# Optimization experiments

Measured on AMD Instinct MI355X. Metric: run time of the kernel, lower is better.

Reference implementation:

```python
import jax, jax.numpy as jnp
import numpy as np

N = 50000        # nodes
E = 1600000      # edges (avg degree 32)
F_IN = 128
F_OUT = 128


def setup_inputs() -> dict:
    key = jax.random.key(0)
    k = jax.random.split(key, 6)
    h = jax.random.normal(k[0], (N, F_IN), dtype=jnp.float32)
    edge_feat = jax.random.normal(k[1], (E,), dtype=jnp.float32)
    src = jax.random.randint(k[2], (E,), 0, N, dtype=jnp.int32)
    dst = jax.random.randint(k[3], (E,), 0, N, dtype=jnp.int32)
    # xavier_uniform with gain=1.414 over fan_in=F_IN, fan_out=F_OUT
    limit = 1.414 * np.sqrt(6.0 / (F_IN + F_OUT))
    weight = jax.random.uniform(k[4], (2, F_IN, F_OUT), minval=-limit, maxval=limit, dtype=jnp.float32)
    std_v = 1.0 / np.sqrt(F_OUT)
    bias = jax.random.uniform(k[5], (F_OUT,), minval=-std_v, maxval=std_v, dtype=jnp.float32)
    return {"h": h, "edge_feat": edge_feat, "src": src, "dst": dst, "weight": weight, "bias": bias}


def reference(h, edge_feat, src, dst, weight, bias):
    # Two linear transforms: [N, F_out] each
    h0 = h @ weight[0]
    h1 = h @ weight[1]
    # F.softmax with no dim on a 1-D edge tensor -> softmax over ALL edges
    e = jax.nn.softmax(edge_feat)                      # [E]
    # update_all(u_mul_e, sum) twice with the SAME edge weights; by linearity
    # scatter(e*h0[src]) + scatter(e*h1[src]) == scatter(e*(h0+h1)[src])
    msg = (h0 + h1)[src] * e[:, None]                  # [E, F_out]
    out = jax.ops.segment_sum(msg, dst, num_segments=N)  # [N, F_out]
    return out + bias
```

## Files before the change

kernel.cpp:

```cpp
#include <hip/hip_runtime.h>
#include <math.h>

#define F 128
#define CAP 2688
#define SCHUNK 6400
#define SCANB 256
typedef unsigned long long ull;
typedef unsigned int uint;
typedef float f32x4 __attribute__((ext_vector_type(4)));
typedef short bf16x8 __attribute__((ext_vector_type(8)));


__device__ __forceinline__ uint fp4_enc(float v) {
    uint s = (__float_as_uint(v) >> 28) & 8u;
    float af = fabsf(v);
    uint c = af < 0.5f ? 0u : af < 1.5f ? 1u : af < 2.5f ? 2u : af < 3.5f ? 3u
           : af < 5.0f ? 4u : af < 7.0f ? 5u : af < 10.0f ? 6u : 7u;
    return s | c;
}

#if __has_builtin(__builtin_amdgcn_cvt_scalef32_pk_f32_fp4)
__device__ __forceinline__ void dec8_fma(uint x, float w, float* acc) {
    auto p0 = __builtin_amdgcn_cvt_scalef32_pk_f32_fp4(x, 2.0f, 0);
    auto p1 = __builtin_amdgcn_cvt_scalef32_pk_f32_fp4(x, 2.0f, 1);
    auto p2 = __builtin_amdgcn_cvt_scalef32_pk_f32_fp4(x, 2.0f, 2);
    auto p3 = __builtin_amdgcn_cvt_scalef32_pk_f32_fp4(x, 2.0f, 3);
    acc[0] += w * p0[0]; acc[1] += w * p0[1];
    acc[2] += w * p1[0]; acc[3] += w * p1[1];
    acc[4] += w * p2[0]; acc[5] += w * p2[1];
    acc[6] += w * p3[0]; acc[7] += w * p3[1];
}
#else
__device__ __forceinline__ uint fp4x4_to_fp8x4(uint b) {
    uint mag = b & 0x07070707u;
    uint sgn = (b & 0x08080808u) << 4;
    uint g2  = ((mag >> 1) | (mag >> 2)) & 0x01010101u;
    uint msk = g2 * 0xFFu;
    uint A   = 0x30303030u + (mag << 2);
    uint B   = (mag & 0x01010101u) * 0x30u;
    return sgn | (msk & A) | (~msk & B);
}
__device__ __forceinline__ void dec8_fma(uint x, float w, float* acc) {
    uint lo = x & 0x0F0F0F0Fu;
    uint hi = (x >> 4) & 0x0F0F0F0Fu;
    uint f8l = fp4x4_to_fp8x4(lo);
    uint f8h = fp4x4_to_fp8x4(hi);
    auto p0 = __builtin_amdgcn_cvt_pk_f32_fp8(f8l, false);
    auto p1 = __builtin_amdgcn_cvt_pk_f32_fp8(f8l, true);
    auto p2 = __builtin_amdgcn_cvt_pk_f32_fp8(f8h, false);
    auto p3 = __builtin_amdgcn_cvt_pk_f32_fp8(f8h, true);
    float w2 = w * 2.0f;
    acc[0] += w2 * p0[0]; acc[2] += w2 * p0[1]; acc[4] += w2 * p1[0]; acc[6] += w2 * p1[1];
    acc[1] += w2 * p2[0]; acc[3] += w2 * p2[1]; acc[5] += w2 * p3[0]; acc[7] += w2 * p3[1];
}
#endif

__device__ __forceinline__ uint pk_bf16(float a, float b) {
    uint ua = __float_as_uint(a); ua = (ua + 0x7FFFu + ((ua >> 16) & 1u)) >> 16;
    uint ub = __float_as_uint(b); ub = (ub + 0x7FFFu + ((ub >> 16) & 1u)) >> 16;
    return ua | (ub << 16);
}

__global__ void k_setup(float* __restrict__ scal, int* __restrict__ bucketCursor,
                        const float* __restrict__ W, unsigned short* __restrict__ WT, int NBK) {
    int i = blockIdx.x * 256 + threadIdx.x;
    if (i < F * F) {
        int k = i >> 7, n = i & 127;
        float v = W[i] + W[F * F + i];
        uint u = __float_as_uint(v);
        u = (u + 0x7FFFu + ((u >> 16) & 1u)) >> 16;
        WT[n * F + k] = (unsigned short)u;
    }
    if (i < 16) scal[i] = 0.0f;
    if (i < NBK) bucketCursor[i] = i * CAP;
}

__global__ __launch_bounds__(1024, 4) void k_main(const float* __restrict__ h,
                                                  const unsigned short* __restrict__ WT,
                                                  unsigned short* __restrict__ hs4, int N,
                                                  const int* __restrict__ src,
                                                  const int* __restrict__ dst,
                                                  const float* __restrict__ ef, int E, int NBK,
                                                  int* __restrict__ bucketCursor,
                                                  ull* __restrict__ ebin,
                                                  float* __restrict__ scal) {
    __shared__ __align__(16) char sm[65536];
    int t = threadIdx.x;

    if (blockIdx.x >= SCANB) {
        char* ldsA = sm;
        int row0 = (int)(blockIdx.x - SCANB) * 256;

        for (int c = t; c < 256 * 16; c += 1024) {
            int r = c >> 4, cc = c & 15;
            float4 v0 = make_float4(0.f, 0.f, 0.f, 0.f), v1 = v0;
            if (row0 + r < N) {
                const float4* hp = (const float4*)(h + (size_t)(row0 + r) * F + cc * 8);
                v0 = hp[0]; v1 = hp[1];
            }
            uint4 b;
            b.x = pk_bf16(v0.x, v0.y); b.y = pk_bf16(v0.z, v0.w);
            b.z = pk_bf16(v1.x, v1.y); b.w = pk_bf16(v1.z, v1.w);
            *(uint4*)(ldsA + (r * 256 + ((cc * 16) ^ ((r & 7) << 4)))) = b;
        }
        __syncthreads();

        int lane = t & 63, wid = t >> 6;
        int lr = lane & 15;
        int kg = lane >> 4;
        int lrow = wid * 16 + lr;

        f32x4 acc[8];
        #pragma unroll
        for (int ct = 0; ct < 8; ++ct) acc[ct] = (f32x4){0.f, 0.f, 0.f, 0.f};

        #pragma unroll
        for (int ks = 0; ks < 4; ++ks) {
            bf16x8 bh = *(const bf16x8*)(ldsA + (lrow * 256 + ((ks * 64 + kg * 16) ^ ((lrow & 7) << 4))));
            #pragma unroll
            for (int ct = 0; ct < 8; ++ct) {
                bf16x8 aw = *(const bf16x8*)(WT + (size_t)(16 * ct + lr) * F + ks * 32 + kg * 8);
                acc[ct] = __builtin_amdgcn_mfma_f32_16x16x32_bf16(aw, bh, acc[ct], 0, 0, 0);
            }
        }
        __syncthreads();

        unsigned short* ldsO = (unsigned short*)sm;
        #pragma unroll
        for (int ct = 0; ct < 8; ++ct) {
            uint c = fp4_enc(acc[ct][0]) | (fp4_enc(acc[ct][1]) << 4)
                   | (fp4_enc(acc[ct][2]) << 8) | (fp4_enc(acc[ct][3]) << 12);
            ldsO[lrow * 32 + 4 * ct + kg] = (unsigned short)c;
        }
        __syncthreads();

        if (row0 + (t >> 2) < N)
            *(uint4*)((char*)hs4 + (size_t)row0 * 64 + t * 16) = ((const uint4*)ldsO)[t];
        return;
    }

    int* cnt    = (int*)sm;
    int* runpos = (int*)(sm + 4096);
    int* sdst   = (int*)(sm + 8192);
    float* smf  = (float*)(sm + 8192 + SCHUNK * 4);

    for (int i = t; i < NBK; i += 1024) cnt[i] = 0;
    __syncthreads();
    int chunk = ((E + SCANB - 1) / SCANB + 3) & ~3;
    bool fits = (chunk <= SCHUNK);
    int e0 = blockIdx.x * chunk, e1 = min(e0 + chunk, E);
    int nv = max(0, e1 - e0) & ~3;

    for (int e = e0 + t * 4; e < e0 + nv; e += 1024 * 4) {
        int4 d4 = *(const int4*)(dst + e);
        if (fits) *(int4*)(sdst + (e - e0)) = d4;
        atomicAdd(&cnt[d4.x >> 6], 1);
        atomicAdd(&cnt[d4.y >> 6], 1);
        atomicAdd(&cnt[d4.z >> 6], 1);
        atomicAdd(&cnt[d4.w >> 6], 1);
    }
    for (int e = e0 + nv + t; e < e1; e += 1024) {
        int d = dst[e];
        if (fits) sdst[e - e0] = d;
        atomicAdd(&cnt[d >> 6], 1);
    }
    __syncthreads();

    for (int i = t; i < NBK; i += 1024) {
        int c = cnt[i];
        runpos[i] = (c > 0) ? atomicAdd(&bucketCursor[i], c) : 0;
    }
    __syncthreads();

    float s = 0.0f;
    for (int e = e0 + t * 4; e < e0 + nv; e += 1024 * 4) {
        int4   d4 = fits ? *(const int4*)(sdst + (e - e0)) : *(const int4*)(dst + e);
        int4   s4 = *(const int4*)(src + e);
        float4 f4 = *(const float4*)(ef + e);
        {
            float w = expf(f4.x); s += w;
            int bk = d4.x >> 6;
            int p = atomicAdd(&runpos[bk], 1);
            if (p < (bk + 1) * CAP)
                ebin[p] = ((ull)(uint)__float_as_int(w) << 32) | ((uint)(d4.x & 63) << 20) | (uint)s4.x;
        }
        {
            float w = expf(f4.y); s += w;
            int bk = d4.y >> 6;
            int p = atomicAdd(&runpos[bk], 1);
            if (p < (bk + 1) * CAP)
                ebin[p] = ((ull)(uint)__float_as_int(w) << 32) | ((uint)(d4.y & 63) << 20) | (uint)s4.y;
        }
        {
            float w = expf(f4.z); s += w;
            int bk = d4.z >> 6;
            int p = atomicAdd(&runpos[bk], 1);
            if (p < (bk + 1) * CAP)
                ebin[p] = ((ull)(uint)__float_as_int(w) << 32) | ((uint)(d4.z & 63) << 20) | (uint)s4.z;
        }
        {
            float w = expf(f4.w); s += w;
            int bk = d4.w >> 6;
            int p = atomicAdd(&runpos[bk], 1);
            if (p < (bk + 1) * CAP)
                ebin[p] = ((ull)(uint)__float_as_int(w) << 32) | ((uint)(d4.w & 63) << 20) | (uint)s4.w;
        }
    }
    for (int e = e0 + nv + t; e < e1; e += 1024) {
        int d = fits ? sdst[e - e0] : dst[e];
        int sv = src[e];
        float w = expf(ef[e]); s += w;
        int bk = d >> 6;
        int p = atomicAdd(&runpos[bk], 1);
        if (p < (bk + 1) * CAP)
            ebin[p] = ((ull)(uint)__float_as_int(w) << 32) | ((uint)(d & 63) << 20) | (uint)sv;
    }

    #pragma unroll
    for (int o = 32; o > 0; o >>= 1) s += __shfl_down(s, o, 64);
    int lane = t & 63, wid = t >> 6;
    if (lane == 0) smf[wid] = s;
    __syncthreads();
    if (wid == 0) {
        float v = (lane < 16) ? smf[lane] : 0.0f;
        #pragma unroll
        for (int o = 8; o > 0; o >>= 1) v += __shfl_down(v, o, 64);
        if (lane == 0) atomicAdd(scal + 1, v);
    }
}

__global__ __launch_bounds__(1024) void k_fused(const int* __restrict__ bucketCursor,
                                                const ull* __restrict__ ebin,
                                                const uint* __restrict__ hs4,
                                                const float* __restrict__ bias,
                                                const float* __restrict__ scal,
                                                float* __restrict__ out, int N) {
    extern __shared__ ull smem[];
    ull* stage  = smem;
    ull* sorted = smem + CAP;
    int* cnt = (int*)(smem + 2 * CAP);
    int* cur = cnt + 64;
    int* seg = cur + 64;
    int b = blockIdx.x;
    int base = b * CAP;
    int m = min(bucketCursor[b] - base, CAP);
    int t = threadIdx.x;
    if (t < 64) cnt[t] = 0;
    __syncthreads();
    for (int i = t; i < m; i += 1024) {
        ull v = __builtin_nontemporal_load(&ebin[base + i]);
        stage[i] = v;
        atomicAdd(&cnt[(uint)(v >> 20) & 63u], 1);
    }
    __syncthreads();
    if (t < 64) {
        int v = cnt[t];
        int sc = v;
        #pragma unroll
        for (int o = 1; o < 64; o <<= 1) {
            int u = __shfl_up(sc, o, 64);
            if (t >= o) sc += u;
        }
        seg[t] = sc;
        cur[t] = sc - v;
    }
    __syncthreads();
    for (int i = t; i < m; i += 1024) {
        ull v = stage[i];
        int dl = (int)((uint)(v >> 20) & 63u);
        int p = atomicAdd(&cur[dl], 1);
        sorted[p] = v;
    }
    __syncthreads();
    int wave = t >> 6, lane = t & 63;
    int dl = wave * 4 + (lane >> 4);
    int g = lane & 15;
    int d = b * 64 + dl;
    int c = cnt[dl];
    int s0 = seg[dl] - c;
    float inv = 1.0f / scal[1];
    float acc[8];
    #pragma unroll
    for (int k = 0; k < 8; ++k) acc[k] = 0.0f;
    int j = 0;
    for (; j + 3 < c; j += 4) {
        ull v0 = sorted[s0 + j];
        ull v1 = sorted[s0 + j + 1];
        ull v2 = sorted[s0 + j + 2];
        ull v3 = sorted[s0 + j + 3];
        uint q0 = hs4[(size_t)(uint)(v0 & 0xfffffu) * 16 + g];
        uint q1 = hs4[(size_t)(uint)(v1 & 0xfffffu) * 16 + g];
        uint q2 = hs4[(size_t)(uint)(v2 & 0xfffffu) * 16 + g];
        uint q3 = hs4[(size_t)(uint)(v3 & 0xfffffu) * 16 + g];
        dec8_fma(q0, __uint_as_float((uint)(v0 >> 32)), acc);
        dec8_fma(q1, __uint_as_float((uint)(v1 >> 32)), acc);
        dec8_fma(q2, __uint_as_float((uint)(v2 >> 32)), acc);
        dec8_fma(q3, __uint_as_float((uint)(v3 >> 32)), acc);
    }
    for (; j < c; ++j) {
        ull v = sorted[s0 + j];
        uint q = hs4[(size_t)(uint)(v & 0xfffffu) * 16 + g];
        float w = __uint_as_float((uint)(v >> 32));
        dec8_fma(q, w, acc);
    }
    if (d < N) {
        const float4* b4 = (const float4*)(bias + g * 8);
        float* o = out + (size_t)d * F + g * 8;
        #pragma unroll
        for (int k = 0; k < 2; ++k) {
            float4 bs = b4[k];
            f32x4 r;
            r.x = bs.x + inv * acc[4 * k + 0];
            r.y = bs.y + inv * acc[4 * k + 1];
            r.z = bs.z + inv * acc[4 * k + 2];
            r.w = bs.w + inv * acc[4 * k + 3];
            __builtin_nontemporal_store(r, (f32x4*)(o + 4 * k));
        }
    }
}

extern "C" void kernel_launch(void* const* d_in, const int* in_sizes, int n_in,
                              void* d_out, int out_size, void* d_ws, size_t ws_size,
                              hipStream_t stream) {
    const float* h    = (const float*)d_in[0];
    const float* ef   = (const float*)d_in[1];
    const int*   src  = (const int*)d_in[2];
    const int*   dst  = (const int*)d_in[3];
    const float* W    = (const float*)d_in[4];
    const float* bias = (const float*)d_in[5];
    float*       out  = (float*)d_out;

    int N = in_sizes[0] / F;
    int E = in_sizes[1];
    int NBK = (N + 63) >> 6;
    int GB  = (N + 255) >> 8;

    char*  base = (char*)d_ws;
    float* scal  = (float*)base;                     base += 16 * sizeof(float);
    unsigned short* WT = (unsigned short*)base;      base += F * F * sizeof(unsigned short);
    ull*   ebin  = (ull*)base;                       base += (size_t)NBK * CAP * sizeof(ull);
    unsigned short* hs4 = (unsigned short*)base;     base += (size_t)N * 64;
    int*   bucketCursor = (int*)base;

    size_t fusedLds = (size_t)2 * CAP * 8 + 3 * 64 * 4;

    hipLaunchKernelGGL(k_setup, dim3(64), dim3(256), 0, stream, scal, bucketCursor, W, WT, NBK);
    hipLaunchKernelGGL(k_main,  dim3(SCANB + GB), dim3(1024), 0, stream,
                       h, WT, hs4, N, src, dst, ef, E, NBK, bucketCursor, ebin, scal);
    hipLaunchKernelGGL(k_fused, dim3(NBK), dim3(1024), fusedLds, stream,
                       bucketCursor, ebin, (const uint*)hs4, bias, scal, out, N);
}
```

Before: 154.9 us.

## Fuse setup, GEMM/scan and aggregation into one cooperative kernel with grid sync

Merges the three launches into a single persistent cooperative kernel of 512 blocks, using grid.sync() between the setup, GEMM+edge-binning, and per-bucket aggregation phases. This removes two kernel launch boundaries and their idle gaps. The scan phase now uses the blocks left after the GEMM blocks (512 - GB), and the aggregation loops over buckets per block. If cooperative launch is unavailable it falls back to three kernels, and the scan always uses 512 blocks with a smaller SCHUNK. Risks are fewer blocks for the scan and binning work and grid-sync overhead, plus limited occupancy from 1024-thread blocks with 64KB LDS each.

```diff
diff --git a/kernel.cpp b/kernel.cpp
--- a/kernel.cpp
+++ b/kernel.cpp
@@ -1,10 +1,13 @@
 #include <hip/hip_runtime.h>
+#include <hip/hip_cooperative_groups.h>
 #include <math.h>
+
+namespace cg = cooperative_groups;
 
 #define F 128
 #define CAP 2688
-#define SCHUNK 6400
-#define SCANB 256
+#define SCHUNK 5120
+#define NBLK 512
 typedef unsigned long long ull;
 typedef unsigned int uint;
 typedef float f32x4 __attribute__((ext_vector_type(4)));
@@ -61,84 +64,78 @@
     return ua | (ub << 16);
 }
 
-__global__ void k_setup(float* __restrict__ scal, int* __restrict__ bucketCursor,
-                        const float* __restrict__ W, unsigned short* __restrict__ WT, int NBK) {
-    int i = blockIdx.x * 256 + threadIdx.x;
-    if (i < F * F) {
-        int k = i >> 7, n = i & 127;
-        float v = W[i] + W[F * F + i];
+__device__ __forceinline__ void dev_setup(int gid, const float* __restrict__ W,
+                                          unsigned short* __restrict__ WT,
+                                          float* __restrict__ scal,
+                                          int* __restrict__ cursor, int NBK) {
+    if (gid < F * F) {
+        int k = gid >> 7, n = gid & 127;
+        float v = W[gid] + W[F * F + gid];
         uint u = __float_as_uint(v);
         u = (u + 0x7FFFu + ((u >> 16) & 1u)) >> 16;
         WT[n * F + k] = (unsigned short)u;
     }
-    if (i < 16) scal[i] = 0.0f;
-    if (i < NBK) bucketCursor[i] = i * CAP;
-}
-
-__global__ __launch_bounds__(1024, 4) void k_main(const float* __restrict__ h,
-                                                  const unsigned short* __restrict__ WT,
-                                                  unsigned short* __restrict__ hs4, int N,
-                                                  const int* __restrict__ src,
-                                                  const int* __restrict__ dst,
-                                                  const float* __restrict__ ef, int E, int NBK,
-                                                  int* __restrict__ bucketCursor,
-                                                  ull* __restrict__ ebin,
-                                                  float* __restrict__ scal) {
-    __shared__ __align__(16) char sm[65536];
-    int t = threadIdx.x;
-
-    if (blockIdx.x >= SCANB) {
-        char* ldsA = sm;
-        int row0 = (int)(blockIdx.x - SCANB) * 256;
-
-        for (int c = t; c < 256 * 16; c += 1024) {
-            int r = c >> 4, cc = c & 15;
-            float4 v0 = make_float4(0.f, 0.f, 0.f, 0.f), v1 = v0;
-            if (row0 + r < N) {
-                const float4* hp = (const float4*)(h + (size_t)(row0 + r) * F + cc * 8);
-                v0 = hp[0]; v1 = hp[1];
-            }
-            uint4 b;
-            b.x = pk_bf16(v0.x, v0.y); b.y = pk_bf16(v0.z, v0.w);
-            b.z = pk_bf16(v1.x, v1.y); b.w = pk_bf16(v1.z, v1.w);
-            *(uint4*)(ldsA + (r * 256 + ((cc * 16) ^ ((r & 7) << 4)))) = b;
-        }
-        __syncthreads();
-
-        int lane = t & 63, wid = t >> 6;
-        int lr = lane & 15;
-        int kg = lane >> 4;
-        int lrow = wid * 16 + lr;
-
-        f32x4 acc[8];
-        #pragma unroll
-        for (int ct = 0; ct < 8; ++ct) acc[ct] = (f32x4){0.f, 0.f, 0.f, 0.f};
-
-        #pragma unroll
-        for (int ks = 0; ks < 4; ++ks) {
-            bf16x8 bh = *(const bf16x8*)(ldsA + (lrow * 256 + ((ks * 64 + kg * 16) ^ ((lrow & 7) << 4))));
-            #pragma unroll
-            for (int ct = 0; ct < 8; ++ct) {
-                bf16x8 aw = *(const bf16x8*)(WT + (size_t)(16 * ct + lr) * F + ks * 32 + kg * 8);
-                acc[ct] = __builtin_amdgcn_mfma_f32_16x16x32_bf16(aw, bh, acc[ct], 0, 0, 0);
-            }
-        }
-        __syncthreads();
-
-        unsigned short* ldsO = (unsigned short*)sm;
+    if (gid < 16) scal[gid] = 0.0f;
+    int ci = gid - F * F;
+    if (ci >= 0 && ci < NBK) cursor[ci] = ci * CAP;
+}
+
+__device__ void dev_gemm(char* sm, int t, int row0, const float* __restrict__ h,
+                         const unsigned short* __restrict__ WT,
+                         unsigned short* __restrict__ hs4, int N) {
+    char* ldsA = sm;
+    for (int c = t; c < 256 * 16; c += 1024) {
+        int r = c >> 4, cc = c & 15;
+        float4 v0 = make_float4(0.f, 0.f, 0.f, 0.f), v1 = v0;
+        if (row0 + r < N) {
+            const float4* hp = (const float4*)(h + (size_t)(row0 + r) * F + cc * 8);
+            v0 = hp[0]; v1 = hp[1];
+        }
+        uint4 b;
+        b.x = pk_bf16(v0.x, v0.y); b.y = pk_bf16(v0.z, v0.w);
+        b.z = pk_bf16(v1.x, v1.y); b.w = pk_bf16(v1.z, v1.w);
+        *(uint4*)(ldsA + (r * 256 + ((cc * 16) ^ ((r & 7) << 4)))) = b;
+    }
+    __syncthreads();
+
+    int lane = t & 63, wid = t >> 6;
+    int lr = lane & 15;
+    int kg = lane >> 4;
+    int lrow = wid * 16 + lr;
+
+    f32x4 acc[8];
+    #pragma unroll
+    for (int ct = 0; ct < 8; ++ct) acc[ct] = (f32x4){0.f, 0.f, 0.f, 0.f};
+
+    #pragma unroll
+    for (int ks = 0; ks < 4; ++ks) {
+        bf16x8 bh = *(const bf16x8*)(ldsA + (lrow * 256 + ((ks * 64 + kg * 16) ^ ((lrow & 7) << 4))));
         #pragma unroll
         for (int ct = 0; ct < 8; ++ct) {
-            uint c = fp4_enc(acc[ct][0]) | (fp4_enc(acc[ct][1]) << 4)
-                   | (fp4_enc(acc[ct][2]) << 8) | (fp4_enc(acc[ct][3]) << 12);
-            ldsO[lrow * 32 + 4 * ct + kg] = (unsigned short)c;
-        }
-        __syncthreads();
-
-        if (row0 + (t >> 2) < N)
-            *(uint4*)((char*)hs4 + (size_t)row0 * 64 + t * 16) = ((const uint4*)ldsO)[t];
-        return;
-    }
-
+            bf16x8 aw = *(const bf16x8*)(WT + (size_t)(16 * ct + lr) * F + ks * 32 + kg * 8);
+            acc[ct] = __builtin_amdgcn_mfma_f32_16x16x32_bf16(aw, bh, acc[ct], 0, 0, 0);
+        }
+    }
+    __syncthreads();
+
+    unsigned short* ldsO = (unsigned short*)sm;
+    #pragma unroll
+    for (int ct = 0; ct < 8; ++ct) {
+        uint c = fp4_enc(acc[ct][0]) | (fp4_enc(acc[ct][1]) << 4)
+               | (fp4_enc(acc[ct][2]) << 8) | (fp4_enc(acc[ct][3]) << 12);
+        ldsO[lrow * 32 + 4 * ct + kg] = (unsigned short)c;
+    }
+    __syncthreads();
+
+    if (row0 + (t >> 2) < N)
+        *(uint4*)((char*)hs4 + (size_t)row0 * 64 + t * 16) = ((const uint4*)sm)[t];
+}
+
+__device__ void dev_scan(char* sm, int t, int bid2, int scanb,
+                         const int* __restrict__ src, const int* __restrict__ dst,
+                         const float* __restrict__ ef, int E, int NBK,
+                         int* __restrict__ cursor, ull* __restrict__ ebin,
+                         float* __restrict__ scal) {
     int* cnt    = (int*)sm;
     int* runpos = (int*)(sm + 4096);
     int* sdst   = (int*)(sm + 8192);
@@ -146,9 +143,9 @@
 
     for (int i = t; i < NBK; i += 1024) cnt[i] = 0;
     __syncthreads();
-    int chunk = ((E + SCANB - 1) / SCANB + 3) & ~3;
+    int chunk = ((E + scanb - 1) / scanb + 3) & ~3;
     bool fits = (chunk <= SCHUNK);
-    int e0 = blockIdx.x * chunk, e1 = min(e0 + chunk, E);
+    int e0 = bid2 * chunk, e1 = min(e0 + chunk, E);
     int nv = max(0, e1 - e0) & ~3;
 
     for (int e = e0 + t * 4; e < e0 + nv; e += 1024 * 4) {
@@ -168,7 +165,7 @@
 
     for (int i = t; i < NBK; i += 1024) {
         int c = cnt[i];
-        runpos[i] = (c > 0) ? atomicAdd(&bucketCursor[i], c) : 0;
+        runpos[i] = (c > 0) ? atomicAdd(&cursor[i], c) : 0;
     }
     __syncthreads();
 
@@ -229,22 +226,18 @@
     }
 }
 
-__global__ __launch_bounds__(1024) void k_fused(const int* __restrict__ bucketCursor,
-                                                const ull* __restrict__ ebin,
-                                                const uint* __restrict__ hs4,
-                                                const float* __restrict__ bias,
-                                                const float* __restrict__ scal,
-                                                float* __restrict__ out, int N) {
-    extern __shared__ ull smem[];
-    ull* stage  = smem;
-    ull* sorted = smem + CAP;
-    int* cnt = (int*)(smem + 2 * CAP);
+__device__ void dev_fused(char* sm, int t, int b, const int* __restrict__ cursor,
+                          const ull* __restrict__ ebin, const uint* __restrict__ hs4,
+                          const float* __restrict__ bias, const float* __restrict__ scal,
+                          float* __restrict__ out, int N) {
+    ull* stage  = (ull*)sm;
+    ull* sorted = stage + CAP;
+    int* cnt = (int*)(sm + 2 * CAP * 8);
     int* cur = cnt + 64;
     int* seg = cur + 64;
-    int b = blockIdx.x;
     int base = b * CAP;
-    int m = min(bucketCursor[b] - base, CAP);
-    int t = threadIdx.x;
+    int m = min(cursor[b] - base, CAP);
+    __syncthreads();
     if (t < 64) cnt[t] = 0;
     __syncthreads();
     for (int i = t; i < m; i += 1024) {
@@ -300,8 +293,7 @@
     for (; j < c; ++j) {
         ull v = sorted[s0 + j];
         uint q = hs4[(size_t)(uint)(v & 0xfffffu) * 16 + g];
-        float w = __uint_as_float((uint)(v >> 32));
-        dec8_fma(q, w, acc);
+        dec8_fma(q, __uint_as_float((uint)(v >> 32)), acc);
     }
     if (d < N) {
         const float4* b4 = (const float4*)(bias + g * 8);
@@ -319,6 +311,57 @@
     }
 }
 
+__global__ __launch_bounds__(1024, 4) void k_mega(const float* __restrict__ h,
+                                                  const float* __restrict__ W,
+                                                  const float* __restrict__ bias,
+                                                  const int* __restrict__ src,
+                                                  const int* __restrict__ dst,
+                                                  const float* __restrict__ ef,
+                                                  float* __restrict__ out,
+                                                  int N, int E, int NBK, int GB,
+                                                  unsigned short* __restrict__ WT,
+                                                  unsigned short* __restrict__ hs4,
+                                                  ull* __restrict__ ebin,
+                                                  int* __restrict__ cursor,
+                                                  float* __restrict__ scal) {
+    __shared__ __align__(16) char sm[65536];
+    cg::grid_group grid = cg::this_grid();
+    int t = threadIdx.x, bid = (int)blockIdx.x;
+
+    dev_setup(bid * 1024 + t, W, WT, scal, cursor, NBK);
+    grid.sync();
+
+    if (bid < GB) dev_gemm(sm, t, bid * 256, h, WT, hs4, N);
+    else          dev_scan(sm, t, bid - GB, NBLK - GB, src, dst, ef, E, NBK, cursor, ebin, scal);
+    grid.sync();
+
+    for (int b = bid; b < NBK; b += NBLK)
+        dev_fused(sm, t, b, cursor, ebin, (const uint*)hs4, bias, scal, out, N);
+}
+
+__global__ void k_setup_f(float* scal, int* cursor, const float* W,
+                          unsigned short* WT, int NBK) {
+    dev_setup((int)blockIdx.x * 256 + (int)threadIdx.x, W, WT, scal, cursor, NBK);
+}
+
+__global__ __launch_bounds__(1024, 4) void k_main_f(const float* h, const unsigned short* WT,
+                                                    unsigned short* hs4, int N, int GB,
+                                                    const int* src, const int* dst,
+                                                    const float* ef, int E, int NBK,
+                                                    int* cursor, ull* ebin, float* scal) {
+    __shared__ __align__(16) char sm[65536];
+    int t = threadIdx.x, bid = (int)blockIdx.x;
+    if (bid < GB) dev_gemm(sm, t, bid * 256, h, WT, hs4, N);
+    else          dev_scan(sm, t, bid - GB, 512, src, dst, ef, E, NBK, cursor, ebin, scal);
+}
+
+__global__ __launch_bounds__(1024) void k_fused_f(const int* cursor, const ull* ebin,
+                                                  const uint* hs4, const float* bias,
+                                                  const float* scal, float* out, int N) {
+    __shared__ __align__(16) char sm[65536];
+    dev_fused(sm, (int)threadIdx.x, (int)blockIdx.x, cursor, ebin, hs4, bias, scal, out, N);
+}
+
 extern "C" void kernel_launch(void* const* d_in, const int* in_sizes, int n_in,
                               void* d_out, int out_size, void* d_ws, size_t ws_size,
                               hipStream_t stream) {
@@ -340,13 +383,28 @@
     unsigned short* WT = (unsigned short*)base;      base += F * F * sizeof(unsigned short);
     ull*   ebin  = (ull*)base;                       base += (size_t)NBK * CAP * sizeof(ull);
     unsigned short* hs4 = (unsigned short*)base;     base += (size_t)N * 64;
-    int*   bucketCursor = (int*)base;
-
-    size_t fusedLds = (size_t)2 * CAP * 8 + 3 * 64 * 4;
-
-    hipLaunchKernelGGL(k_setup, dim3(64), dim3(256), 0, stream, scal, bucketCursor, W, WT, NBK);
-    hipLaunchKernelGGL(k_main,  dim3(SCANB + GB), dim3(1024), 0, stream,
-                       h, WT, hs4, N, src, dst, ef, E, NBK, bucketCursor, ebin, scal);
-    hipLaunchKernelGGL(k_fused, dim3(NBK), dim3(1024), fusedLds, stream,
-                       bucketCursor, ebin, (const uint*)hs4, bias, scal, out, N);
-}
+    int*   cursor = (int*)base;
+
+    bool coop = false;
+    int maxb = 0;
+    if (hipOccupancyMaxActiveBlocksPerMultiprocessor(&maxb, (const void*)k_mega, 1024, 0)
+            == hipSuccess && maxb >= 2) {
+        void* args[] = {(void*)&h, (void*)&W, (void*)&bias, (void*)&src, (void*)&dst,
+                        (void*)&ef, (void*)&out, (void*)&N, (void*)&E, (void*)&NBK,
+                        (void*)&GB, (void*)&WT, (void*)&hs4, (void*)&ebin,
+                        (void*)&cursor, (void*)&scal};
+        if (hipLaunchCooperativeKernel((const void*)k_mega, dim3(NBLK), dim3(1024),
+                                       args, 0, stream) == hipSuccess)
+            coop = true;
+        else
+            (void)hipGetLastError();
+    }
+    if (!coop) {
+        hipLaunchKernelGGL(k_setup_f, dim3((F * F + NBK + 255) / 256), dim3(256), 0, stream,
+                           scal, cursor, W, WT, NBK);
+        hipLaunchKernelGGL(k_main_f, dim3(GB + 512), dim3(1024), 0, stream,
+                           h, WT, hs4, N, GB, src, dst, ef, E, NBK, cursor, ebin, scal);
+        hipLaunchKernelGGL(k_fused_f, dim3(NBK), dim3(1024), 0, stream,
+                           cursor, ebin, (const uint*)hs4, bias, scal, out, N);
+    }
+}
```

Measured after the change: 153.5 us. Within noise of the previous version (-0.9%).
